# Performance work log

Hardware: AMD Instinct MI355X
Metric: run time of the kernel (lower is better)

The kernel has to match this reference:

```python
import jax, jax.numpy as jnp
import numpy as np

B = 32768
N_SPARSE = 26
N_DENSE = 13
VOCAB = 10000
E = 64
H = 2
L = 3
DH = E // H
DNN_IN = N_DENSE + N_SPARSE * E  # 1677
H1, H2 = 256, 128


def setup_inputs() -> dict:
    key = jax.random.key(0)
    ks = jax.random.split(key, 12)
    sparse_idx = jax.random.randint(ks[0], (B, N_SPARSE), 0, VOCAB, dtype=jnp.int32)
    dense = jax.random.uniform(ks[1], (B, N_DENSE), dtype=jnp.float32)
    X = jnp.concatenate([sparse_idx.astype(jnp.float32), dense], axis=1)  # [B,39]
    emb_tables = jax.random.normal(ks[2], (N_SPARSE, VOCAB, E), dtype=jnp.float32)
    Wq = jax.random.normal(ks[3], (L, E, E), dtype=jnp.float32) * 0.05
    Wk = jax.random.normal(ks[4], (L, E, E), dtype=jnp.float32) * 0.05
    Wv = jax.random.normal(ks[5], (L, E, E), dtype=jnp.float32) * 0.05
    Wres = jax.random.normal(ks[6], (L, E, E), dtype=jnp.float32) * 0.05
    dnn_W1 = jax.random.normal(ks[7], (DNN_IN, H1), dtype=jnp.float32) * 1e-4
    dnn_b1 = jnp.zeros((H1,), dtype=jnp.float32)
    dnn_W2 = jax.random.normal(ks[8], (H1, H2), dtype=jnp.float32) * 1e-4
    dnn_b2 = jnp.zeros((H2,), dtype=jnp.float32)
    out_W = jax.random.normal(ks[9], (N_SPARSE * E + H2, 1), dtype=jnp.float32) * 1e-5
    lin_W = jax.random.normal(ks[10], (N_SPARSE + N_DENSE, 1), dtype=jnp.float32) * 1e-5
    lin_b = jnp.zeros((1,), dtype=jnp.float32)
    return {"X": X, "sparse_idx": sparse_idx, "emb_tables": emb_tables,
            "Wq": Wq, "Wk": Wk, "Wv": Wv, "Wres": Wres,
            "dnn_W1": dnn_W1, "dnn_b1": dnn_b1, "dnn_W2": dnn_W2, "dnn_b2": dnn_b2,
            "out_W": out_W, "lin_W": lin_W, "lin_b": lin_b}


def _split_heads(x):
    # torch.stack(torch.split(x, DH, dim=2)) -> [H, B, F, DH]
    b, f, _ = x.shape
    return jnp.moveaxis(x.reshape(b, f, H, DH), 2, 0)


def _interacting_layer(att, wq, wk, wv, wres):
    # att: [B, F, E]
    q = _split_heads(jnp.einsum('bfe,eo->bfo', att, wq))  # [H,B,F,DH]
    k = _split_heads(jnp.einsum('bfe,eo->bfo', att, wk))
    v = _split_heads(jnp.einsum('bfe,eo->bfo', att, wv))
    scores = jnp.einsum('hbik,hbjk->hbij', q, k)           # [H,B,F,F] (no scaling: default scaling=False)
    attn = jax.nn.softmax(scores, axis=-1)
    out = jnp.einsum('hbij,hbjd->hbid', attn, v)           # [H,B,F,DH]
    b, f = att.shape[0], att.shape[1]
    out = jnp.moveaxis(out, 0, 2).reshape(b, f, E)         # cat heads along last dim
    out = out + jnp.einsum('bfe,eo->bfo', att, wres)       # residual (use_res=True)
    return jax.nn.relu(out)


def reference(X, sparse_idx, emb_tables, Wq, Wk, Wv, Wres,
              dnn_W1, dnn_b1, dnn_W2, dnn_b2, out_W, lin_W, lin_b):
    # linear logit tower (dropout in eval mode -> identity)
    logit = jax.nn.relu(X @ lin_W + lin_b)                 # [B,1]
    # embedding gather: table f indexed by sparse_idx[:,f]
    emb = emb_tables[jnp.arange(N_SPARSE), sparse_idx]     # [B, F, E]
    att = emb
    for l in range(L):
        att = _interacting_layer(att, Wq[l], Wk[l], Wv[l], Wres[l])
    att_flat = att.reshape(att.shape[0], -1)               # [B, F*E]
    sparse_flat = emb.reshape(emb.shape[0], -1)            # [B, F*E]
    dense_input = X[:, N_SPARSE:]                          # [B, 13]
    dnn_in = jnp.concatenate([dense_input, sparse_flat], axis=1)
    h = jax.nn.relu(dnn_in @ dnn_W1 + dnn_b1)
    h = jax.nn.relu(h @ dnn_W2 + dnn_b2)
    stack = jnp.concatenate([att_flat, h], axis=-1)
    logit = logit + stack @ out_W
    return jax.nn.sigmoid(logit)
```

## Files before the change

### kernel.cpp

```cpp
#include <hip/hip_runtime.h>
#include <math.h>

#define BATCH 32768
#define NSP 26
#define NDN 13
#define VOC 10000
#define EDIM 64
#define NLAY 3
#define HID1 256
#define HID2 128
#define XW 39
#define KCH 27

typedef short short8 __attribute__((ext_vector_type(8)));
typedef float float4v __attribute__((ext_vector_type(4)));

__device__ __forceinline__ unsigned short f2b(float f) {
    unsigned u = __builtin_bit_cast(unsigned, f);
    u += 0x7FFFu + ((u >> 16) & 1u);
    return (unsigned short)(u >> 16);
}
__device__ __forceinline__ float b2f(unsigned short h) {
    unsigned u = ((unsigned)h) << 16;
    return __builtin_bit_cast(float, u);
}
__device__ __forceinline__ unsigned pk2(float lo, float hi) {
    unsigned ul = __builtin_bit_cast(unsigned, lo);
    unsigned uh = __builtin_bit_cast(unsigned, hi);
    ul += 0x7FFFu + ((ul >> 16) & 1u);
    uh += 0x7FFFu + ((uh >> 16) & 1u);
    return (uh & 0xFFFF0000u) | (ul >> 16);
}
__device__ __forceinline__ uint2 pkC(float4v c) {
    uint2 r; r.x = pk2(c[0], c[1]); r.y = pk2(c[2], c[3]); return r;
}
__device__ __forceinline__ void st4(unsigned short* p, float4v v) {
    *(uint2*)p = pkC(v);
}
__device__ __forceinline__ short8 cat(uint2 a, uint2 b) {
    union { unsigned u[4]; short8 s; } r;
    r.u[0] = a.x; r.u[1] = a.y; r.u[2] = b.x; r.u[3] = b.y;
    return r.s;
}

__global__ void k_pack(const float* __restrict__ Wq, const float* __restrict__ Wk,
                       const float* __restrict__ Wv, const float* __restrict__ Wr,
                       const float* __restrict__ W1, const float* __restrict__ W2,
                       unsigned short* __restrict__ pW,
                       unsigned short* __restrict__ pW1,
                       unsigned short* __restrict__ pW2) {
    int bid = blockIdx.x;
    if (bid < 192) {
        int tid = bid * 256 + threadIdx.x;
        int j    = tid & 7;
        int lane = (tid >> 3) & 63;
        int kt   = (tid >> 9) & 1;
        int nt   = (tid >> 10) & 3;
        int m    = (tid >> 12) & 3;
        int l    = tid >> 14;
        const float* W = (m == 0) ? Wq : (m == 1) ? Wk : (m == 2) ? Wv : Wr;
        int k = kt * 32 + ((lane >> 4) << 3) + j;
        int n = nt * 16 + (lane & 15);
        pW[tid] = f2b(W[l * EDIM * EDIM + k * EDIM + n]);
    } else if (bid < 1920) {
        int tid = (bid - 192) * 256 + threadIdx.x;
        int j    = tid & 7;
        int lane = (tid >> 3) & 63;
        int nt   = (tid >> 9) & 15;
        int rest = tid >> 13;
        int kt = rest & 1, c = rest >> 1;
        int kl = kt * 32 + ((lane >> 4) << 3) + j;
        int n  = nt * 16 + (lane & 15);
        int row;
        if (c < NSP) row = 13 + c * 64 + kl;
        else         row = (kl < NDN) ? kl : -1;
        pW1[tid] = (row >= 0) ? f2b(W1[(long)row * HID1 + n]) : (unsigned short)0;
    } else {
        int tid = (bid - 1920) * 256 + threadIdx.x;
        int j    = tid & 7;
        int lane = (tid >> 3) & 63;
        int nt   = (tid >> 9) & 7;
        int kc   = tid >> 12;
        int k = kc * 32 + ((lane >> 4) << 3) + j;
        int n = nt * 16 + (lane & 15);
        pW2[tid] = f2b(W2[(long)k * HID2 + n]);
    }
}

__global__ void k_lin(const float* __restrict__ X, const float* __restrict__ lw,
                      const float* __restrict__ lb, float* __restrict__ logit0) {
    int b = blockIdx.x * 256 + threadIdx.x;
    float s = lb[0];
    const float* xr = X + (long)b * XW;
#pragma unroll
    for (int i = 0; i < XW; i++) s = fmaf(xr[i], lw[i], s);
    logit0[b] = fmaxf(s, 0.f);
}

__global__ __launch_bounds__(64, 3) void k_interact(
    const int* __restrict__ sidx, const float* __restrict__ emb,
    const unsigned short* __restrict__ pW, const float* __restrict__ outW,
    float* __restrict__ p1)
{
    __shared__ __align__(16) unsigned short att[32 * 72];

    const int lane = threadIdx.x;
    const int b    = blockIdx.x;
    const int quad = lane >> 4;
    const int c16  = lane & 15;
    const float4v zero4 = {0.f, 0.f, 0.f, 0.f};

#pragma unroll
    for (int f = 0; f < NSP; f++) {
        int idx = sidx[b * NSP + f];
        att[f * 72 + lane] = f2b(emb[((long)(f * VOC + idx)) * EDIM + lane]);
    }
#pragma unroll
    for (int r = NSP; r < 32; r++) att[r * 72 + lane] = 0;
    __syncthreads();

    for (int l = 0; l < NLAY; l++) {
        short8 Fatt[2][2];
#pragma unroll
        for (int qt = 0; qt < 2; qt++)
#pragma unroll
            for (int kt = 0; kt < 2; kt++)
                Fatt[qt][kt] = *(const short8*)&att[(qt*16 + c16)*72 + kt*32 + quad*8];

        const unsigned short* wl = pW + l * 16384;
        uint2 qpk[4][2];
        uint2 kpk[4][2];
        uint2 vpk[2][4];
        uint2 rpk[4][2];

#pragma unroll
        for (int m = 0; m < 4; m++) {
            short8 Wf[4][2];
#pragma unroll
            for (int nt = 0; nt < 4; nt++)
#pragma unroll
                for (int kt = 0; kt < 2; kt++)
                    Wf[nt][kt] = *(const short8*)&wl[(m*8 + nt*2 + kt)*512 + lane*8];

            if (m == 2) {
#pragma unroll
                for (int qt = 0; qt < 2; qt++)
#pragma unroll
                    for (int dt = 0; dt < 4; dt++) {
                        float4v acc = __builtin_amdgcn_mfma_f32_16x16x32_bf16(
                            Fatt[qt][0], Wf[dt][0], zero4, 0, 0, 0);
                        acc = __builtin_amdgcn_mfma_f32_16x16x32_bf16(
                            Fatt[qt][1], Wf[dt][1], acc, 0, 0, 0);
                        vpk[qt][dt] = pkC(acc);
                    }
            } else {
#pragma unroll
                for (int dt = 0; dt < 4; dt++)
#pragma unroll
                    for (int qt = 0; qt < 2; qt++) {
                        float4v acc = __builtin_amdgcn_mfma_f32_16x16x32_bf16(
                            Wf[dt][0], Fatt[qt][0], zero4, 0, 0, 0);
                        acc = __builtin_amdgcn_mfma_f32_16x16x32_bf16(
                            Wf[dt][1], Fatt[qt][1], acc, 0, 0, 0);
                        if (m == 0)      qpk[dt][qt] = pkC(acc);
                        else if (m == 1) kpk[dt][qt] = pkC(acc);
                        else             rpk[dt][qt] = pkC(acc);
                    }
            }
        }

        uint2 Ppk[2][2][2];
#pragma unroll
        for (int h = 0; h < 2; h++)
#pragma unroll
            for (int nq = 0; nq < 2; nq++) {
                short8 Qc = cat(qpk[h*2][nq], qpk[h*2+1][nq]);
                float4v S0 = __builtin_amdgcn_mfma_f32_16x16x32_bf16(
                    cat(kpk[h*2][0], kpk[h*2+1][0]), Qc, zero4, 0, 0, 0);
                float4v S1 = __builtin_amdgcn_mfma_f32_16x16x32_bf16(
                    cat(kpk[h*2][1], kpk[h*2+1][1]), Qc, zero4, 0, 0, 0);
                float sv[8];
#pragma unroll
                for (int r = 0; r < 4; r++) {
                    sv[r]     = S0[r];
                    sv[4 + r] = (quad*4 + r >= 10) ? -1e30f : S1[r];
                }
                float mx = sv[0];
#pragma unroll
                for (int j = 1; j < 8; j++) mx = fmaxf(mx, sv[j]);
                mx = fmaxf(mx, __shfl_xor(mx, 16));
                mx = fmaxf(mx, __shfl_xor(mx, 32));
                float e[8], sum = 0.f;
#pragma unroll
                for (int j = 0; j < 8; j++) {
                    e[j] = (j >= 4 && quad*4 + (j-4) >= 10) ? 0.f : __expf(sv[j] - mx);
                    sum += e[j];
                }
                sum += __shfl_xor(sum, 16);
                sum += __shfl_xor(sum, 32);
                float inv = 1.f / sum;
                Ppk[h][0][nq].x = pk2(e[0]*inv, e[1]*inv);
                Ppk[h][0][nq].y = pk2(e[2]*inv, e[3]*inv);
                Ppk[h][1][nq].x = pk2(e[4]*inv, e[5]*inv);
                Ppk[h][1][nq].y = pk2(e[6]*inv, e[7]*inv);
            }

#pragma unroll
        for (int h = 0; h < 2; h++)
#pragma unroll
            for (int md = 0; md < 2; md++) {
                int dt = h*2 + md;
                short8 Vc = cat(vpk[0][dt], vpk[1][dt]);
#pragma unroll
                for (int nq = 0; nq < 2; nq++) {
                    float4v O = __builtin_amdgcn_mfma_f32_16x16x32_bf16(
                        Vc, cat(Ppk[h][0][nq], Ppk[h][1][nq]), zero4, 0, 0, 0);
                    uint2 rp = rpk[dt][nq];
                    float4v o;
                    o[0] = fmaxf(O[0] + b2f((unsigned short)(rp.x & 0xFFFF)), 0.f);
                    o[1] = fmaxf(O[1] + b2f((unsigned short)(rp.x >> 16)),   0.f);
                    o[2] = fmaxf(O[2] + b2f((unsigned short)(rp.y & 0xFFFF)), 0.f);
                    o[3] = fmaxf(O[3] + b2f((unsigned short)(rp.y >> 16)),   0.f);
                    st4(&att[(nq*16 + c16)*72 + dt*16 + quad*4], o);
                }
            }
        __syncthreads();
    }

    float s = 0.f;
#pragma unroll
    for (int f = 0; f < NSP; f++)
        s = fmaf(b2f(att[f*72 + lane]), outW[f*EDIM + lane], s);
#pragma unroll
    for (int off = 32; off > 0; off >>= 1) s += __shfl_down(s, off);
    if (lane == 0) p1[b] = s;
}

__global__ __launch_bounds__(256) void k_dnn(
    const float* __restrict__ X, const int* __restrict__ sidx,
    const float* __restrict__ emb, const unsigned short* __restrict__ pW1,
    const float* __restrict__ b1, const unsigned short* __restrict__ pW2,
    const float* __restrict__ b2, const float* __restrict__ outW,
    const float* __restrict__ logit0, const float* __restrict__ p1,
    float* __restrict__ out)
{
    __shared__ __align__(16) unsigned short smem[64 * 264];
    unsigned short* Abuf  = smem;
    unsigned short* h1buf = smem;
    unsigned short* h2buf = smem;

    const int t    = threadIdx.x;
    const int lane = t & 63;
    const int w    = t >> 6;
    const int quad = lane >> 4;
    const int c16  = lane & 15;
    const int bM   = blockIdx.x * 64;
    const int sr   = t >> 2;
    const int part = t & 3;

    float4v acc[4][4];
#pragma unroll
    for (int mt = 0; mt < 4; mt++)
#pragma unroll
        for (int nt = 0; nt < 4; nt++) acc[mt][nt] = (float4v){0.f, 0.f, 0.f, 0.f};

    for (int c = 0; c < KCH; c++) {
        if (c < NSP) {
            int idx = sidx[(bM + sr) * NSP + c];
            const float4* src = (const float4*)(emb + ((long)(c * VOC + idx)) * EDIM + part * 16);
            float4 a = src[0], bb = src[1], cc = src[2], dd = src[3];
            uint4 w0 = { pk2(a.x,a.y),  pk2(a.z,a.w),  pk2(bb.x,bb.y), pk2(bb.z,bb.w) };
            uint4 w1 = { pk2(cc.x,cc.y), pk2(cc.z,cc.w), pk2(dd.x,dd.y), pk2(dd.z,dd.w) };
            *(uint4*)&Abuf[sr * 72 + part * 16]     = w0;
            *(uint4*)&Abuf[sr * 72 + part * 16 + 8] = w1;
        } else {
            unsigned short v[16];
#pragma unroll
            for (int i = 0; i < 16; i++) {
                int j = part * 16 + i;
                v[i] = (j < NDN) ? f2b(X[(long)(bM + sr) * XW + NSP + j])
                                 : (unsigned short)0;
            }
            *(uint4*)&Abuf[sr * 72 + part * 16]     = *(uint4*)&v[0];
            *(uint4*)&Abuf[sr * 72 + part * 16 + 8] = *(uint4*)&v[8];
        }
        __syncthreads();

#pragma unroll
        for (int kt = 0; kt < 2; kt++) {
            short8 Bf[4], Af[4];
#pragma unroll
            for (int nt = 0; nt < 4; nt++)
                Bf[nt] = *(const short8*)&pW1[((long)((c*2 + kt)*16 + w*4 + nt) * 64 + lane) * 8];
#pragma unroll
            for (int mt = 0; mt < 4; mt++)
                Af[mt] = *(const short8*)&Abuf[(mt*16 + c16)*72 + kt*32 + quad*8];
#pragma unroll
            for (int mt = 0; mt < 4; mt++)
#pragma unroll
                for (int nt = 0; nt < 4; nt++)
                    acc[mt][nt] = __builtin_amdgcn_mfma_f32_16x16x32_bf16(
                        Af[mt], Bf[nt], acc[mt][nt], 0, 0, 0);
        }
        __syncthreads();
    }

#pragma unroll
    for (int nt = 0; nt < 4; nt++) {
        int n = w * 64 + nt * 16 + c16;
        float bias = b1[n];
#pragma unroll
        for (int mt = 0; mt < 4; mt++)
#pragma unroll
            for (int reg = 0; reg < 4; reg++)
                h1buf[(mt * 16 + quad * 4 + reg) * 264 + n] =
                    f2b(fmaxf(acc[mt][nt][reg] + bias, 0.f));
    }
    __syncthreads();

    float4v acc2[4][2];
#pragma unroll
    for (int mt = 0; mt < 4; mt++)
#pragma unroll
        for (int n2 = 0; n2 < 2; n2++) acc2[mt][n2] = (float4v){0.f, 0.f, 0.f, 0.f};
#pragma unroll
    for (int kc2 = 0; kc2 < 8; kc2++) {
        short8 Bf2[2], Af2[4];
#pragma unroll
        for (int n2 = 0; n2 < 2; n2++)
            Bf2[n2] = *(const short8*)&pW2[((kc2 * 8 + w * 2 + n2) * 64 + lane) * 8];
#pragma unroll
        for (int mt = 0; mt < 4; mt++)
            Af2[mt] = *(const short8*)&h1buf[(mt * 16 + c16) * 264 + kc2 * 32 + quad * 8];
#pragma unroll
        for (int mt = 0; mt < 4; mt++)
#pragma unroll
            for (int n2 = 0; n2 < 2; n2++)
                acc2[mt][n2] = __builtin_amdgcn_mfma_f32_16x16x32_bf16(
                    Af2[mt], Bf2[n2], acc2[mt][n2], 0, 0, 0);
    }
    __syncthreads();

#pragma unroll
    for (int n2 = 0; n2 < 2; n2++) {
        int n = w * 32 + n2 * 16 + c16;
        float bias = b2[n];
#pragma unroll
        for (int mt = 0; mt < 4; mt++)
#pragma unroll
            for (int reg = 0; reg < 4; reg++)
                h2buf[(mt * 16 + quad * 4 + reg) * 136 + n] =
                    f2b(fmaxf(acc2[mt][n2][reg] + bias, 0.f));
    }
    __syncthreads();

    if (t < 64) {
        const float* ow2 = outW + NSP * EDIM;
        float s = 0.f;
#pragma unroll
        for (int c8 = 0; c8 < 16; c8++) {
            short8 h = *(const short8*)&h2buf[t * 136 + c8 * 8];
#pragma unroll
            for (int j = 0; j < 8; j++)
                s = fmaf(b2f((unsigned short)h[j]), ow2[c8 * 8 + j], s);
        }
        int bb = bM + t;
        float logit = logit0[bb] + p1[bb] + s;
        out[bb] = 1.f / (1.f + __expf(-logit));
    }
}

extern "C" void kernel_launch(void* const* d_in, const int* in_sizes, int n_in,
                              void* d_out, int out_size, void* d_ws, size_t ws_size,
                              hipStream_t stream) {
    const float* X    = (const float*)d_in[0];
    const int*   sidx = (const int*)d_in[1];
    const float* emb  = (const float*)d_in[2];
    const float* Wq   = (const float*)d_in[3];
    const float* Wk   = (const float*)d_in[4];
    const float* Wv   = (const float*)d_in[5];
    const float* Wres = (const float*)d_in[6];
    const float* W1   = (const float*)d_in[7];
    const float* b1   = (const float*)d_in[8];
    const float* W2   = (const float*)d_in[9];
    const float* b2   = (const float*)d_in[10];
    const float* outW = (const float*)d_in[11];
    const float* linW = (const float*)d_in[12];
    const float* linb = (const float*)d_in[13];
    float* out = (float*)d_out;

    float* logit0 = (float*)d_ws;
    float* p1     = logit0 + BATCH;
    unsigned short* pW  = (unsigned short*)(p1 + BATCH);
    unsigned short* pW1 = pW + 49152;
    unsigned short* pW2 = pW1 + 442368;

    k_pack<<<2048, 256, 0, stream>>>(Wq, Wk, Wv, Wres, W1, W2, pW, pW1, pW2);
    k_lin<<<BATCH / 256, 256, 0, stream>>>(X, linW, linb, logit0);
    k_interact<<<BATCH, 64, 0, stream>>>(sidx, emb, pW, outW, p1);
    k_dnn<<<BATCH / 64, 256, 0, stream>>>(X, sidx, emb, pW1, b1, pW2, b2, outW,
                                          logit0, p1, out);
}
```

Before: 380.3 us.

## Switch MFMA math from bf16 to fp16 and pack four samples per interact block

Every bf16 conversion and MFMA is replaced with fp16. Conversion now uses the hardware packed round-toward-zero instruction instead of manual integer round-to-nearest-even bit tricks, which cuts ALU work in the conversion-heavy paths. Separately, k_interact now runs four independent 64-lane waves per 256-thread block, each with its own shared buffer. Block-wide barriers become block fences. This reduces block count and per-block launch overhead, at the risk of fp16 range limits and a weaker intra-wave LDS ordering guarantee.

New measurement: 769.2 us. 102% more time.

```diff
diff --git a/kernel.cpp b/kernel.cpp
--- a/kernel.cpp
+++ b/kernel.cpp
@@ -12,35 +12,30 @@
 #define XW 39
 #define KCH 27
 
-typedef short short8 __attribute__((ext_vector_type(8)));
-typedef float float4v __attribute__((ext_vector_type(4)));
-
-__device__ __forceinline__ unsigned short f2b(float f) {
-    unsigned u = __builtin_bit_cast(unsigned, f);
-    u += 0x7FFFu + ((u >> 16) & 1u);
-    return (unsigned short)(u >> 16);
-}
-__device__ __forceinline__ float b2f(unsigned short h) {
-    unsigned u = ((unsigned)h) << 16;
-    return __builtin_bit_cast(float, u);
-}
-__device__ __forceinline__ unsigned pk2(float lo, float hi) {
-    unsigned ul = __builtin_bit_cast(unsigned, lo);
-    unsigned uh = __builtin_bit_cast(unsigned, hi);
-    ul += 0x7FFFu + ((ul >> 16) & 1u);
-    uh += 0x7FFFu + ((uh >> 16) & 1u);
-    return (uh & 0xFFFF0000u) | (ul >> 16);
+typedef __fp16   fp16x2 __attribute__((ext_vector_type(2)));
+typedef _Float16 half8  __attribute__((ext_vector_type(8)));
+typedef float float4v   __attribute__((ext_vector_type(4)));
+
+__device__ __forceinline__ unsigned pkh(float lo, float hi) {
+    fp16x2 h = __builtin_amdgcn_cvt_pkrtz(lo, hi);
+    return __builtin_bit_cast(unsigned, h);
+}
+__device__ __forceinline__ unsigned short f2h(float f) {
+    return __builtin_bit_cast(unsigned short, (_Float16)f);
+}
+__device__ __forceinline__ float h2f(unsigned short h) {
+    return (float)__builtin_bit_cast(_Float16, h);
 }
 __device__ __forceinline__ uint2 pkC(float4v c) {
-    uint2 r; r.x = pk2(c[0], c[1]); r.y = pk2(c[2], c[3]); return r;
+    uint2 r; r.x = pkh(c[0], c[1]); r.y = pkh(c[2], c[3]); return r;
 }
 __device__ __forceinline__ void st4(unsigned short* p, float4v v) {
     *(uint2*)p = pkC(v);
 }
-__device__ __forceinline__ short8 cat(uint2 a, uint2 b) {
-    union { unsigned u[4]; short8 s; } r;
+__device__ __forceinline__ half8 cat(uint2 a, uint2 b) {
+    union { unsigned u[4]; half8 h; } r;
     r.u[0] = a.x; r.u[1] = a.y; r.u[2] = b.x; r.u[3] = b.y;
-    return r.s;
+    return r.h;
 }
 
 __global__ void k_pack(const float* __restrict__ Wq, const float* __restrict__ Wk,
@@ -61,7 +56,7 @@
         const float* W = (m == 0) ? Wq : (m == 1) ? Wk : (m == 2) ? Wv : Wr;
         int k = kt * 32 + ((lane >> 4) << 3) + j;
         int n = nt * 16 + (lane & 15);
-        pW[tid] = f2b(W[l * EDIM * EDIM + k * EDIM + n]);
+        pW[tid] = f2h(W[l * EDIM * EDIM + k * EDIM + n]);
     } else if (bid < 1920) {
         int tid = (bid - 192) * 256 + threadIdx.x;
         int j    = tid & 7;
@@ -74,7 +69,7 @@
         int row;
         if (c < NSP) row = 13 + c * 64 + kl;
         else         row = (kl < NDN) ? kl : -1;
-        pW1[tid] = (row >= 0) ? f2b(W1[(long)row * HID1 + n]) : (unsigned short)0;
+        pW1[tid] = (row >= 0) ? f2h(W1[(long)row * HID1 + n]) : (unsigned short)0;
     } else {
         int tid = (bid - 1920) * 256 + threadIdx.x;
         int j    = tid & 7;
@@ -83,7 +78,7 @@
         int kc   = tid >> 12;
         int k = kc * 32 + ((lane >> 4) << 3) + j;
         int n = nt * 16 + (lane & 15);
-        pW2[tid] = f2b(W2[(long)k * HID2 + n]);
+        pW2[tid] = f2h(W2[(long)k * HID2 + n]);
     }
 }
 
@@ -97,15 +92,18 @@
     logit0[b] = fmaxf(s, 0.f);
 }
 
-__global__ __launch_bounds__(64, 3) void k_interact(
+__global__ __launch_bounds__(256, 8) void k_interact(
     const int* __restrict__ sidx, const float* __restrict__ emb,
     const unsigned short* __restrict__ pW, const float* __restrict__ outW,
     float* __restrict__ p1)
 {
-    __shared__ __align__(16) unsigned short att[32 * 72];
-
-    const int lane = threadIdx.x;
-    const int b    = blockIdx.x;
+    __shared__ __align__(16) unsigned short att_s[4][32 * 72];
+
+    const int wid  = threadIdx.x >> 6;
+    const int lane = threadIdx.x & 63;
+    const int b    = blockIdx.x * 4 + wid;
+    unsigned short* att = att_s[wid];
+
     const int quad = lane >> 4;
     const int c16  = lane & 15;
     const float4v zero4 = {0.f, 0.f, 0.f, 0.f};
@@ -113,19 +111,19 @@
 #pragma unroll
     for (int f = 0; f < NSP; f++) {
         int idx = sidx[b * NSP + f];
-        att[f * 72 + lane] = f2b(emb[((long)(f * VOC + idx)) * EDIM + lane]);
+        att[f * 72 + lane] = f2h(emb[((long)(f * VOC + idx)) * EDIM + lane]);
     }
 #pragma unroll
     for (int r = NSP; r < 32; r++) att[r * 72 + lane] = 0;
-    __syncthreads();
+    __threadfence_block();
 
     for (int l = 0; l < NLAY; l++) {
-        short8 Fatt[2][2];
+        half8 Fatt[2][2];
 #pragma unroll
         for (int qt = 0; qt < 2; qt++)
 #pragma unroll
             for (int kt = 0; kt < 2; kt++)
-                Fatt[qt][kt] = *(const short8*)&att[(qt*16 + c16)*72 + kt*32 + quad*8];
+                Fatt[qt][kt] = *(const half8*)&att[(qt*16 + c16)*72 + kt*32 + quad*8];
 
         const unsigned short* wl = pW + l * 16384;
         uint2 qpk[4][2];
@@ -135,21 +133,21 @@
 
 #pragma unroll
         for (int m = 0; m < 4; m++) {
-            short8 Wf[4][2];
+            half8 Wf[4][2];
 #pragma unroll
             for (int nt = 0; nt < 4; nt++)
 #pragma unroll
                 for (int kt = 0; kt < 2; kt++)
-                    Wf[nt][kt] = *(const short8*)&wl[(m*8 + nt*2 + kt)*512 + lane*8];
+                    Wf[nt][kt] = *(const half8*)&wl[(m*8 + nt*2 + kt)*512 + lane*8];
 
             if (m == 2) {
 #pragma unroll
                 for (int qt = 0; qt < 2; qt++)
 #pragma unroll
                     for (int dt = 0; dt < 4; dt++) {
-                        float4v acc = __builtin_amdgcn_mfma_f32_16x16x32_bf16(
+                        float4v acc = __builtin_amdgcn_mfma_f32_16x16x32_f16(
                             Fatt[qt][0], Wf[dt][0], zero4, 0, 0, 0);
-                        acc = __builtin_amdgcn_mfma_f32_16x16x32_bf16(
+                        acc = __builtin_amdgcn_mfma_f32_16x16x32_f16(
                             Fatt[qt][1], Wf[dt][1], acc, 0, 0, 0);
                         vpk[qt][dt] = pkC(acc);
                     }
@@ -158,9 +156,9 @@
                 for (int dt = 0; dt < 4; dt++)
 #pragma unroll
                     for (int qt = 0; qt < 2; qt++) {
-                        float4v acc = __builtin_amdgcn_mfma_f32_16x16x32_bf16(
+                        float4v acc = __builtin_amdgcn_mfma_f32_16x16x32_f16(
                             Wf[dt][0], Fatt[qt][0], zero4, 0, 0, 0);
-                        acc = __builtin_amdgcn_mfma_f32_16x16x32_bf16(
+                        acc = __builtin_amdgcn_mfma_f32_16x16x32_f16(
                             Wf[dt][1], Fatt[qt][1], acc, 0, 0, 0);
                         if (m == 0)      qpk[dt][qt] = pkC(acc);
                         else if (m == 1) kpk[dt][qt] = pkC(acc);
@@ -174,10 +172,10 @@
         for (int h = 0; h < 2; h++)
 #pragma unroll
             for (int nq = 0; nq < 2; nq++) {
-                short8 Qc = cat(qpk[h*2][nq], qpk[h*2+1][nq]);
-                float4v S0 = __builtin_amdgcn_mfma_f32_16x16x32_bf16(
+                half8 Qc = cat(qpk[h*2][nq], qpk[h*2+1][nq]);
+                float4v S0 = __builtin_amdgcn_mfma_f32_16x16x32_f16(
                     cat(kpk[h*2][0], kpk[h*2+1][0]), Qc, zero4, 0, 0, 0);
-                float4v S1 = __builtin_amdgcn_mfma_f32_16x16x32_bf16(
+                float4v S1 = __builtin_amdgcn_mfma_f32_16x16x32_f16(
                     cat(kpk[h*2][1], kpk[h*2+1][1]), Qc, zero4, 0, 0, 0);
                 float sv[8];
 #pragma unroll
@@ -199,10 +197,10 @@
                 sum += __shfl_xor(sum, 16);
                 sum += __shfl_xor(sum, 32);
                 float inv = 1.f / sum;
-                Ppk[h][0][nq].x = pk2(e[0]*inv, e[1]*inv);
-                Ppk[h][0][nq].y = pk2(e[2]*inv, e[3]*inv);
-                Ppk[h][1][nq].x = pk2(e[4]*inv, e[5]*inv);
-                Ppk[h][1][nq].y = pk2(e[6]*inv, e[7]*inv);
+                Ppk[h][0][nq].x = pkh(e[0]*inv, e[1]*inv);
+                Ppk[h][0][nq].y = pkh(e[2]*inv, e[3]*inv);
+                Ppk[h][1][nq].x = pkh(e[4]*inv, e[5]*inv);
+                Ppk[h][1][nq].y = pkh(e[6]*inv, e[7]*inv);
             }
 
 #pragma unroll
@@ -210,27 +208,27 @@
 #pragma unroll
             for (int md = 0; md < 2; md++) {
                 int dt = h*2 + md;
-                short8 Vc = cat(vpk[0][dt], vpk[1][dt]);
+                half8 Vc = cat(vpk[0][dt], vpk[1][dt]);
 #pragma unroll
                 for (int nq = 0; nq < 2; nq++) {
-                    float4v O = __builtin_amdgcn_mfma_f32_16x16x32_bf16(
+                    float4v O = __builtin_amdgcn_mfma_f32_16x16x32_f16(
                         Vc, cat(Ppk[h][0][nq], Ppk[h][1][nq]), zero4, 0, 0, 0);
                     uint2 rp = rpk[dt][nq];
                     float4v o;
-                    o[0] = fmaxf(O[0] + b2f((unsigned short)(rp.x & 0xFFFF)), 0.f);
-                    o[1] = fmaxf(O[1] + b2f((unsigned short)(rp.x >> 16)),   0.f);
-                    o[2] = fmaxf(O[2] + b2f((unsigned short)(rp.y & 0xFFFF)), 0.f);
-                    o[3] = fmaxf(O[3] + b2f((unsigned short)(rp.y >> 16)),   0.f);
+                    o[0] = fmaxf(O[0] + h2f((unsigned short)(rp.x & 0xFFFF)), 0.f);
+                    o[1] = fmaxf(O[1] + h2f((unsigned short)(rp.x >> 16)),   0.f);
+                    o[2] = fmaxf(O[2] + h2f((unsigned short)(rp.y & 0xFFFF)), 0.f);
+                    o[3] = fmaxf(O[3] + h2f((unsigned short)(rp.y >> 16)),   0.f);
                     st4(&att[(nq*16 + c16)*72 + dt*16 + quad*4], o);
                 }
             }
-        __syncthreads();
+        __threadfence_block();
     }
 
     float s = 0.f;
 #pragma unroll
     for (int f = 0; f < NSP; f++)
-        s = fmaf(b2f(att[f*72 + lane]), outW[f*EDIM + lane], s);
+        s = fmaf(h2f(att[f*72 + lane]), outW[f*EDIM + lane], s);
 #pragma unroll
     for (int off = 32; off > 0; off >>= 1) s += __shfl_down(s, off);
     if (lane == 0) p1[b] = s;
@@ -269,8 +267,8 @@
             int idx = sidx[(bM + sr) * NSP + c];
             const float4* src = (const float4*)(emb + ((long)(c * VOC + idx)) * EDIM + part * 16);
             float4 a = src[0], bb = src[1], cc = src[2], dd = src[3];
-            uint4 w0 = { pk2(a.x,a.y),  pk2(a.z,a.w),  pk2(bb.x,bb.y), pk2(bb.z,bb.w) };
-            uint4 w1 = { pk2(cc.x,cc.y), pk2(cc.z,cc.w), pk2(dd.x,dd.y), pk2(dd.z,dd.w) };
+            uint4 w0 = { pkh(a.x,a.y),   pkh(a.z,a.w),   pkh(bb.x,bb.y), pkh(bb.z,bb.w) };
+            uint4 w1 = { pkh(cc.x,cc.y), pkh(cc.z,cc.w), pkh(dd.x,dd.y), pkh(dd.z,dd.w) };
             *(uint4*)&Abuf[sr * 72 + part * 16]     = w0;
             *(uint4*)&Abuf[sr * 72 + part * 16 + 8] = w1;
         } else {
@@ -278,7 +276,7 @@
 #pragma unroll
             for (int i = 0; i < 16; i++) {
                 int j = part * 16 + i;
-                v[i] = (j < NDN) ? f2b(X[(long)(bM + sr) * XW + NSP + j])
+                v[i] = (j < NDN) ? f2h(X[(long)(bM + sr) * XW + NSP + j])
                                  : (unsigned short)0;
             }
             *(uint4*)&Abuf[sr * 72 + part * 16]     = *(uint4*)&v[0];
@@ -288,18 +286,18 @@
 
 #pragma unroll
         for (int kt = 0; kt < 2; kt++) {
-            short8 Bf[4], Af[4];
+            half8 Bf[4], Af[4];
 #pragma unroll
             for (int nt = 0; nt < 4; nt++)
-                Bf[nt] = *(const short8*)&pW1[((long)((c*2 + kt)*16 + w*4 + nt) * 64 + lane) * 8];
+                Bf[nt] = *(const half8*)&pW1[((long)((c*2 + kt)*16 + w*4 + nt) * 64 + lane) * 8];
 #pragma unroll
             for (int mt = 0; mt < 4; mt++)
-                Af[mt] = *(const short8*)&Abuf[(mt*16 + c16)*72 + kt*32 + quad*8];
+                Af[mt] = *(const half8*)&Abuf[(mt*16 + c16)*72 + kt*32 + quad*8];
 #pragma unroll
             for (int mt = 0; mt < 4; mt++)
 #pragma unroll
                 for (int nt = 0; nt < 4; nt++)
-                    acc[mt][nt] = __builtin_amdgcn_mfma_f32_16x16x32_bf16(
+                    acc[mt][nt] = __builtin_amdgcn_mfma_f32_16x16x32_f16(
                         Af[mt], Bf[nt], acc[mt][nt], 0, 0, 0);
         }
         __syncthreads();
@@ -314,7 +312,7 @@
 #pragma unroll
             for (int reg = 0; reg < 4; reg++)
                 h1buf[(mt * 16 + quad * 4 + reg) * 264 + n] =
-                    f2b(fmaxf(acc[mt][nt][reg] + bias, 0.f));
+                    f2h(fmaxf(acc[mt][nt][reg] + bias, 0.f));
     }
     __syncthreads();
 
@@ -325,18 +323,18 @@
         for (int n2 = 0; n2 < 2; n2++) acc2[mt][n2] = (float4v){0.f, 0.f, 0.f, 0.f};
 #pragma unroll
     for (int kc2 = 0; kc2 < 8; kc2++) {
-        short8 Bf2[2], Af2[4];
+        half8 Bf2[2], Af2[4];
 #pragma unroll
         for (int n2 = 0; n2 < 2; n2++)
-            Bf2[n2] = *(const short8*)&pW2[((kc2 * 8 + w * 2 + n2) * 64 + lane) * 8];
+            Bf2[n2] = *(const half8*)&pW2[((kc2 * 8 + w * 2 + n2) * 64 + lane) * 8];
 #pragma unroll
         for (int mt = 0; mt < 4; mt++)
-            Af2[mt] = *(const short8*)&h1buf[(mt * 16 + c16) * 264 + kc2 * 32 + quad * 8];
+            Af2[mt] = *(const half8*)&h1buf[(mt * 16 + c16) * 264 + kc2 * 32 + quad * 8];
 #pragma unroll
         for (int mt = 0; mt < 4; mt++)
 #pragma unroll
             for (int n2 = 0; n2 < 2; n2++)
-                acc2[mt][n2] = __builtin_amdgcn_mfma_f32_16x16x32_bf16(
+                acc2[mt][n2] = __builtin_amdgcn_mfma_f32_16x16x32_f16(
                     Af2[mt], Bf2[n2], acc2[mt][n2], 0, 0, 0);
     }
     __syncthreads();
@@ -350,7 +348,7 @@
 #pragma unroll
             for (int reg = 0; reg < 4; reg++)
                 h2buf[(mt * 16 + quad * 4 + reg) * 136 + n] =
-                    f2b(fmaxf(acc2[mt][n2][reg] + bias, 0.f));
+                    f2h(fmaxf(acc2[mt][n2][reg] + bias, 0.f));
     }
     __syncthreads();
 
@@ -359,10 +357,10 @@
         float s = 0.f;
 #pragma unroll
         for (int c8 = 0; c8 < 16; c8++) {
-            short8 h = *(const short8*)&h2buf[t * 136 + c8 * 8];
+            half8 h = *(const half8*)&h2buf[t * 136 + c8 * 8];
 #pragma unroll
             for (int j = 0; j < 8; j++)
-                s = fmaf(b2f((unsigned short)h[j]), ow2[c8 * 8 + j], s);
+                s = fmaf((float)h[j], ow2[c8 * 8 + j], s);
         }
         int bb = bM + t;
         float logit = logit0[bb] + p1[bb] + s;
@@ -397,7 +395,7 @@
 
     k_pack<<<2048, 256, 0, stream>>>(Wq, Wk, Wv, Wres, W1, W2, pW, pW1, pW2);
     k_lin<<<BATCH / 256, 256, 0, stream>>>(X, linW, linb, logit0);
-    k_interact<<<BATCH, 64, 0, stream>>>(sidx, emb, pW, outW, p1);
+    k_interact<<<BATCH / 4, 256, 0, stream>>>(sidx, emb, pW, outW, p1);
     k_dnn<<<BATCH / 64, 256, 0, stream>>>(X, sidx, emb, pW1, b1, pW2, b2, outW,
                                           logit0, p1, out);
 }
```
